# Performance work log

Measured on AMD Instinct MI355X. Metric: run time of the kernel, lower is better.

## Reference

```python
import jax, jax.numpy as jnp
import numpy as np

B, P, C = 2, 512, 21          # images, proposals/image, classes (incl background)
REG = 5                       # xc, yc, w, h, angle(deg)
DET = 100                     # detections_per_img
IMW, IMH = 1024, 800
SCORE_THRESH = 0.05
NMS_THR = 0.5
WEIGHTS = (10.0, 10.0, 5.0, 5.0, 3.0)
BBOX_XFORM_CLIP = float(np.log(1000.0 / 16.0))
MAXV = 8                      # max vertices of quad-quad intersection


def setup_inputs() -> dict:
    key = jax.random.key(0)
    k1, k2, k3 = jax.random.split(key, 3)
    class_logits = jax.random.normal(k1, (B * P, C), jnp.float32)
    box_regression = jax.random.normal(k2, (B * P, C * REG), jnp.float32)
    u = jax.random.uniform(k3, (B * P, 5), jnp.float32)
    rrects = jnp.stack([
        u[:, 0] * IMW,            # xc
        u[:, 1] * IMH,            # yc
        u[:, 2] * 200.0 + 16.0,   # w
        u[:, 3] * 200.0 + 16.0,   # h
        u[:, 4] * 360.0 - 180.0,  # angle in degrees
    ], axis=1)
    return {"class_logits": class_logits, "box_regression": box_regression, "rrects": rrects}


def rect_pts(r):
    # r [..., 5] -> corner points [..., 4, 2] (CCW quad in math coords)
    xc, yc, w, h, ang = (r[..., i] for i in range(5))
    t = ang * (jnp.pi / 180.0)
    c, s = jnp.cos(t), jnp.sin(t)
    dx, dy = w * 0.5, h * 0.5
    ox = jnp.stack([-dx, dx, dx, -dx], -1)
    oy = jnp.stack([-dy, -dy, dy, dy], -1)
    x = xc[..., None] + c[..., None] * ox - s[..., None] * oy
    y = yc[..., None] + s[..., None] * ox + c[..., None] * oy
    return jnp.stack([x, y], -1)


def decode(deltas, anchors):
    # BoxCoder.decode for rotated boxes, weights (wx,wy,ww,wh,wa)
    d = deltas.reshape(-1, C, REG) / jnp.asarray(WEIGHTS, deltas.dtype)
    dx, dy, dw, dh, da = (d[..., i] for i in range(REG))
    dw = jnp.minimum(dw, BBOX_XFORM_CLIP)
    dh = jnp.minimum(dh, BBOX_XFORM_CLIP)
    xc, yc, w, h, a = (anchors[:, i:i + 1] for i in range(5))
    px = dx * w + xc
    py = dy * h + yc
    pw = jnp.exp(dw) * w
    ph = jnp.exp(dh) * h
    pa = da * (180.0 / jnp.pi) + a
    return jnp.stack([px, py, pw, ph, pa], -1)  # [N, C, 5]


def _clip_edge(poly, n, a, b):
    # Sutherland-Hodgman clip of convex poly (buffer [MAXV,2], count n) by halfplane left of a->b
    d = b - a
    out = jnp.zeros((MAXV, 2), poly.dtype)
    m = jnp.int32(0)
    nn = jnp.maximum(n, 1)
    for i in range(MAXV):
        act = i < n
        s = poly[i]
        e = poly[jnp.mod(i + 1, nn)]
        cs = d[0] * (s[1] - a[1]) - d[1] * (s[0] - a[0])
        ce = d[0] * (e[1] - a[1]) - d[1] * (e[0] - a[0])
        denom = cs - ce
        t = cs / jnp.where(jnp.abs(denom) > 1e-12, denom, 1e-12)
        ip = s + t * (e - s)
        s_in = cs >= 0
        e_in = ce >= 0
        app1 = act & (s_in != e_in)           # crossing -> intersection point
        out = out.at[m].set(jnp.where(app1, ip, out[m]))
        m = m + app1.astype(jnp.int32)
        app2 = act & e_in                     # end point inside -> keep it
        out = out.at[m].set(jnp.where(app2, e, out[m]))
        m = m + app2.astype(jnp.int32)
    return out, m


def inter_area(p1, p2):
    # exact intersection area of two convex quads [4,2]
    poly = jnp.zeros((MAXV, 2), p1.dtype).at[:4].set(p1)
    n = jnp.int32(4)
    for k in range(4):
        poly, n = _clip_edge(poly, n, p2[k], p2[(k + 1) % 4])
    idx = jnp.arange(MAXV)
    nn = jnp.maximum(n, 1)
    nxt = jnp.mod(idx + 1, nn)
    cross = poly[:, 0] * poly[nxt, 1] - poly[nxt, 0] * poly[:, 1]
    area = 0.5 * jnp.abs(jnp.sum(jnp.where(idx < n, cross, 0.0)))
    return jnp.where(n >= 3, area, 0.0)


def _nms_one(args):
    # greedy rotated NMS on one (image,class) score-sorted set
    rr, valid = args                       # [P,5], [P] bool (sorted by desc score)
    pts = rect_pts(rr)                     # [P,4,2]
    areas = rr[:, 2] * rr[:, 3]
    inter = jax.vmap(lambda p: jax.vmap(lambda q: inter_area(p, q))(pts))(pts)
    iou = inter / (areas[:, None] + areas[None, :] - inter + 1e-8)
    n = rr.shape[0]
    def body(i, keep):
        sup = jnp.any(keep & (iou[i] > NMS_THR))
        return keep.at[i].set(valid[i] & jnp.logical_not(sup))
    return jax.lax.fori_loop(0, n, body, jnp.zeros((n,), bool))


def reference(class_logits, box_regression, rrects):
    scores = jax.nn.softmax(class_logits, -1)           # [N,C]
    proposals = decode(box_regression, rrects)          # [N,C,5]
    pts = rect_pts(proposals)                           # [N,C,4,2]
    mn, mx = pts.min(-2), pts.max(-2)
    bb = jnp.concatenate([mn, mx], -1)                  # xyxy [N,C,4]
    bb = jnp.stack([
        jnp.clip(bb[..., 0], 0.0, IMW - 1.0),
        jnp.clip(bb[..., 1], 0.0, IMH - 1.0),
        jnp.clip(bb[..., 2], 0.0, IMW - 1.0),
        jnp.clip(bb[..., 3], 0.0, IMH - 1.0),
    ], -1)

    # per-image, foreground classes only; [B, C-1, P, ...]
    sc = scores.reshape(B, P, C)[:, :, 1:].transpose(0, 2, 1)
    pr = proposals.reshape(B, P, C, 5)[:, :, 1:].transpose(0, 2, 1, 3)
    bx = bb.reshape(B, P, C, 4)[:, :, 1:].transpose(0, 2, 1, 3)

    valid = sc > SCORE_THRESH
    masked = jnp.where(valid, sc, -1.0)
    order = jnp.argsort(-masked, axis=-1)               # desc score per class
    sc_s = jnp.take_along_axis(masked, order, -1)
    valid_s = jnp.take_along_axis(valid, order, -1)
    pr_s = jnp.take_along_axis(pr, order[..., None], 2)
    bx_s = jnp.take_along_axis(bx, order[..., None], 2)

    keep = jax.lax.map(_nms_one, (jax.lax.stop_gradient(pr_s).reshape(-1, P, 5),
                                  valid_s.reshape(-1, P))).reshape(B, C - 1, P)
    keep = jax.lax.stop_gradient(keep)

    msk = jnp.where(keep, sc_s, -1.0)
    flat_s = msk.reshape(B, -1)                         # [B,(C-1)*P]
    top_idx = jax.lax.top_k(flat_s, DET)[1]
    sel_s = jnp.take_along_axis(flat_s, top_idx, -1)
    ok = sel_s > 0.0
    sel_bb = jnp.take_along_axis(bx_s.reshape(B, -1, 4), top_idx[..., None], 1)
    sel_rr = jnp.take_along_axis(pr_s.reshape(B, -1, 5), top_idx[..., None], 1)
    lab = jnp.broadcast_to(jnp.arange(1, C, dtype=jnp.int32)[:, None], (C - 1, P)).reshape(-1)
    sel_lab = lab[top_idx]

    out_bb = jnp.where(ok[..., None], sel_bb, 0.0)
    out_rr = jnp.where(ok[..., None], sel_rr, 0.0)
    out_sc = jnp.where(ok, sel_s, 0.0)
    out_lab = jnp.where(ok, sel_lab, 0)
    return out_bb, out_rr, out_sc, out_lab
```

## Files before the change

kernel.cpp:

```cpp
#include <hip/hip_runtime.h>
#include <stdint.h>

#pragma clang fp contract(off)

#define B_ 2
#define P_ 512
#define C_ 21
#define CF 20
#define DET 100
#define SCORE_THRESH 0.05f
#define NMS_THR 0.5f
#define BBOX_CLIP 4.135166556742356f
#define NC (CF * DET)

typedef unsigned long long u64;
typedef unsigned int u32;

__device__ __forceinline__ u32 f2o(float f) {
  u32 u = __float_as_uint(f);
  return (u & 0x80000000u) ? ~u : (u | 0x80000000u);
}
__device__ __forceinline__ float o2f(u32 o) {
  u32 u = (o & 0x80000000u) ? (o ^ 0x80000000u) : ~o;
  return __uint_as_float(u);
}

__global__ void __launch_bounds__(256)
prep_kernel(const float* __restrict__ logits,
            const float* __restrict__ breg,
            const float* __restrict__ rrects,
            float* __restrict__ scsS,
            float* __restrict__ ptsS,
            float* __restrict__ aabbS,
            float* __restrict__ pr5S,
            float* __restrict__ areaS,
            int* __restrict__ gV,
            u64* __restrict__ sup) {
  int g = blockIdx.x;
  int b = g / CF, cf = g % CF, c = cf + 1;
  int tid = threadIdx.x;

  __shared__ u64 lkey[P_];
  __shared__ int cnt;
  if (tid == 0) cnt = 0;

  u64 kreg[2];
  float fx[2][4], fy[2][4];
  float fab[2][4];
  float fp5[2][5];
  float far_[2];
  float fsc[2];
  #pragma unroll
  for (int e = 0; e < 2; ++e) {
    int p = tid + e * 256;
    int n = b * P_ + p;
    const float* lg = logits + n * C_;
    float mx = lg[0];
    for (int k = 1; k < C_; ++k) mx = fmaxf(mx, lg[k]);
    float den = 0.f;
    for (int k = 0; k < C_; ++k) den += expf(lg[k] - mx);
    float sc = expf(lg[c] - mx) / den;

    const float* d = breg + n * (C_ * 5) + c * 5;
    float dx = d[0] / 10.0f, dy = d[1] / 10.0f;
    float dw = d[2] / 5.0f, dh = d[3] / 5.0f, da = d[4] / 3.0f;
    dw = fminf(dw, BBOX_CLIP);
    dh = fminf(dh, BBOX_CLIP);
    const float* an = rrects + n * 5;
    float px = dx * an[2] + an[0];
    float py = dy * an[3] + an[1];
    float pw = expf(dw) * an[2];
    float ph = expf(dh) * an[3];
    float pa = da * 57.29577951308232f + an[4];
    fp5[e][0] = px; fp5[e][1] = py; fp5[e][2] = pw; fp5[e][3] = ph; fp5[e][4] = pa;
    far_[e] = pw * ph;

    float t = pa * 0.017453292519943295f;
    float cs = cosf(t), sn = sinf(t);
    float hx = pw * 0.5f, hy = ph * 0.5f;
    float ox[4] = {-hx, hx, hx, -hx};
    float oy[4] = {-hy, -hy, hy, hy};
    float minx = 1e30f, miny = 1e30f, maxx = -1e30f, maxy = -1e30f;
    #pragma unroll
    for (int qq = 0; qq < 4; ++qq) {
      float x = px + cs * ox[qq] - sn * oy[qq];
      float y = py + sn * ox[qq] + cs * oy[qq];
      fx[e][qq] = x; fy[e][qq] = y;
      minx = fminf(minx, x); maxx = fmaxf(maxx, x);
      miny = fminf(miny, y); maxy = fmaxf(maxy, y);
    }
    fab[e][0] = minx; fab[e][1] = miny; fab[e][2] = maxx; fab[e][3] = maxy;

    bool valid = sc > SCORE_THRESH;
    float v = valid ? sc : -1.0f;
    fsc[e] = v;
    u64 key = ((u64)f2o(v) << 32) | (u32)(~(u32)p);
    lkey[p] = key;
    kreg[e] = key;
    u64 m = __ballot(valid);
    if ((tid & 63) == 0) atomicAdd(&cnt, __popcll(m));
  }
  for (int w = tid; w < P_ * 8; w += 256) sup[(size_t)g * P_ * 8 + w] = 0ull;
  __syncthreads();

  u64 k0 = kreg[0], k1 = kreg[1];
  int r0 = 0, r1 = 0;
  for (int s = 0; s < P_; ++s) {
    u64 ks = lkey[s];
    r0 += (ks > k0) ? 1 : 0;
    r1 += (ks > k1) ? 1 : 0;
  }
  #pragma unroll
  for (int e = 0; e < 2; ++e) {
    if (fsc[e] > 0.f) {
      int r = (e == 0) ? r0 : r1;
      int so = g * P_ + r;
      scsS[so] = fsc[e];
      ((float4*)ptsS)[so * 2]     = make_float4(fx[e][0], fx[e][1], fx[e][2], fx[e][3]);
      ((float4*)ptsS)[so * 2 + 1] = make_float4(fy[e][0], fy[e][1], fy[e][2], fy[e][3]);
      ((float4*)aabbS)[so] = make_float4(fab[e][0], fab[e][1], fab[e][2], fab[e][3]);
      pr5S[so * 5 + 0] = fp5[e][0]; pr5S[so * 5 + 1] = fp5[e][1];
      pr5S[so * 5 + 2] = fp5[e][2]; pr5S[so * 5 + 3] = fp5[e][3];
      pr5S[so * 5 + 4] = fp5[e][4];
      areaS[so] = far_[e];
    }
  }
  if (tid == 0) gV[g] = cnt;
}

__device__ __forceinline__ float inter_area_reg(const float qx[4], const float qy[4],
                                                const float rx[4], const float ry[4]) {
  float px_[8], py_[8];
  #pragma unroll
  for (int t = 0; t < 8; ++t) { px_[t] = (t < 4) ? qx[t] : 0.f; py_[t] = (t < 4) ? qy[t] : 0.f; }
  int n = 4;
  #pragma unroll
  for (int e = 0; e < 4; ++e) {
    float a0 = rx[e], a1 = ry[e];
    float b0 = rx[(e + 1) & 3], b1 = ry[(e + 1) & 3];
    float dx = b0 - a0, dy = b1 - a1;
    float ox_[8], oy_[8];
    #pragma unroll
    for (int t = 0; t < 8; ++t) { ox_[t] = 0.f; oy_[t] = 0.f; }
    float cr[8];
    #pragma unroll
    for (int t = 0; t < 8; ++t) cr[t] = dx * (py_[t] - a1) - dy * (px_[t] - a0);
    int m = 0;
    int nn = (n > 1) ? n : 1;
    #pragma unroll
    for (int t = 0; t < 8; ++t) {
      bool act = t < n;
      float sx = px_[t], sy = py_[t];
      float ex, ey, ce;
      if (t == 7) { ex = px_[0]; ey = py_[0]; ce = cr[0]; }
      else {
        bool wrap = (t + 1 == nn);
        ex = wrap ? px_[0] : px_[t + 1];
        ey = wrap ? py_[0] : py_[t + 1];
        ce = wrap ? cr[0] : cr[t + 1];
      }
      float cs = cr[t];
      float denom = cs - ce;
      float dn = (fabsf(denom) > 1e-12f) ? denom : 1e-12f;
      float tt = cs / dn;
      float ipx = sx + tt * (ex - sx);
      float ipy = sy + tt * (ey - sy);
      bool s_in = cs >= 0.f, e_in = ce >= 0.f;
      bool app1 = act && (s_in != e_in);
      #pragma unroll
      for (int s2 = 0; s2 < 8; ++s2) {
        bool wr = app1 && (m == s2);
        ox_[s2] = wr ? ipx : ox_[s2];
        oy_[s2] = wr ? ipy : oy_[s2];
      }
      m += app1 ? 1 : 0;
      bool app2 = act && e_in;
      #pragma unroll
      for (int s2 = 0; s2 < 8; ++s2) {
        bool wr = app2 && (m == s2);
        ox_[s2] = wr ? ex : ox_[s2];
        oy_[s2] = wr ? ey : oy_[s2];
      }
      m += app2 ? 1 : 0;
    }
    n = m;
    #pragma unroll
    for (int t = 0; t < 8; ++t) { px_[t] = ox_[t]; py_[t] = oy_[t]; }
  }
  int nn = (n > 1) ? n : 1;
  float s = 0.f;
  #pragma unroll
  for (int t = 0; t < 8; ++t) {
    if (t < n) {
      float nx_x, nx_y;
      if (t == 7) { nx_x = px_[0]; nx_y = py_[0]; }
      else {
        bool wrap = (t + 1 == nn);
        nx_x = wrap ? px_[0] : px_[t + 1];
        nx_y = wrap ? py_[0] : py_[t + 1];
      }
      s += px_[t] * nx_y - nx_x * py_[t];
    }
  }
  float area = 0.5f * fabsf(s);
  return (n >= 3) ? area : 0.f;
}

#define PPT 4
#define TPB 256
__global__ void pair_kernel(const int* __restrict__ gV,
                            const float* __restrict__ aabbS,
                            const float* __restrict__ areaS,
                            const float* __restrict__ ptsS,
                            u64* __restrict__ sup) {
  int g = blockIdx.y;
  int V = gV[g];
  int Tp = V * (V - 1) / 2;
  int base = blockIdx.x * (TPB * PPT);
  if (base >= Tp) return;
  __shared__ u32 q[TPB * PPT];
  __shared__ int qn;
  int tid = threadIdx.x;
  if (tid == 0) qn = 0;
  __syncthreads();
  const float4* ab = (const float4*)aabbS;
  for (int t = 0; t < PPT; ++t) {
    int kk = base + t * TPB + tid;
    if (kk >= Tp) break;
    float kf = (float)kk;
    int i = (int)((1.0f + sqrtf(1.0f + 8.0f * kf)) * 0.5f);
    while (i * (i - 1) / 2 > kk) --i;
    while ((i + 1) * i / 2 <= kk) ++i;
    int j = kk - i * (i - 1) / 2;
    float4 bi = ab[g * P_ + i];
    float4 bj = ab[g * P_ + j];
    bool ov = (bi.x <= bj.z) && (bj.x <= bi.z) && (bi.y <= bj.w) && (bj.y <= bi.w);
    if (ov) {
      int s = atomicAdd(&qn, 1);
      q[s] = (u32)((i << 9) | j);
    }
  }
  __syncthreads();
  int nq = qn;
  const float4* pS = (const float4*)ptsS;
  for (int s = tid; s < nq; s += TPB) {
    u32 pk = q[s];
    int i = (int)(pk >> 9), j = (int)(pk & 511);
    float4 ax = pS[(g * P_ + i) * 2];
    float4 ay = pS[(g * P_ + i) * 2 + 1];
    float4 bx = pS[(g * P_ + j) * 2];
    float4 by = pS[(g * P_ + j) * 2 + 1];
    float qx[4] = {ax.x, ax.y, ax.z, ax.w};
    float qy[4] = {ay.x, ay.y, ay.z, ay.w};
    float rx[4] = {bx.x, bx.y, bx.z, bx.w};
    float ry[4] = {by.x, by.y, by.z, by.w};
    float ai = areaS[g * P_ + i];
    float aj = areaS[g * P_ + j];
    float inter = inter_area_reg(qx, qy, rx, ry);
    float iou = inter / (((ai + aj) - inter) + 1e-8f);
    if (iou > NMS_THR)
      atomicOr(&sup[((size_t)g * P_ + i) * 8 + (j >> 6)], 1ull << (j & 63));
  }
}

__global__ void greedy_kernel(const float* __restrict__ scsS, const int* __restrict__ gV,
                              const float* __restrict__ aabbS, const float* __restrict__ pr5S,
                              const u64* __restrict__ sup,
                              u64* __restrict__ cand, float* __restrict__ rec) {
  int g = blockIdx.x;
  int tid = threadIdx.x;
  __shared__ u64 lsup[P_ * 8];
  __shared__ u32 skeep[16];
  int V = gV[g];
  for (int w = tid; w < V * 8; w += 64) lsup[w] = sup[(size_t)g * P_ * 8 + w];
  __syncthreads();
  u64 keepw = 0;
  u64 cur = (tid < 8 && V > 0) ? lsup[tid] : 0ull;
  for (int i = 0; i < V; ++i) {
    u64 nxt = (tid < 8 && (i + 1) < V) ? lsup[(i + 1) * 8 + tid] : 0ull;
    bool supd = __any((cur & keepw) != 0ull);
    if (!supd && tid == (i >> 6)) keepw |= 1ull << (i & 63);
    cur = nxt;
  }
  if (tid < 8) { skeep[tid * 2] = (u32)keepw; skeep[tid * 2 + 1] = (u32)(keepw >> 32); }
  __syncthreads();
  int cls = g % CF;
  int tot = 0;
  #pragma unroll
  for (int t = 0; t < 16; ++t) tot += __popc(skeep[t]);
  for (int r = tid; r < V; r += 64) {
    if ((skeep[r >> 5] >> (r & 31)) & 1u) {
      int slot = __popc(skeep[r >> 5] & ((1u << (r & 31)) - 1u));
      for (int t = 0; t < (r >> 5); ++t) slot += __popc(skeep[t]);
      if (slot < DET) {
        float sv = scsS[g * P_ + r];
        int flat = cls * P_ + r;
        cand[g * DET + slot] = ((u64)f2o(sv) << 32) | (u32)(~(u32)flat);
        int so = g * P_ + r;
        float* rr = rec + (size_t)(g * DET + slot) * 12;
        rr[0] = fminf(fmaxf(aabbS[so * 4 + 0], 0.f), 1023.0f);
        rr[1] = fminf(fmaxf(aabbS[so * 4 + 1], 0.f), 799.0f);
        rr[2] = fminf(fmaxf(aabbS[so * 4 + 2], 0.f), 1023.0f);
        rr[3] = fminf(fmaxf(aabbS[so * 4 + 3], 0.f), 799.0f);
        rr[4] = pr5S[so * 5 + 0]; rr[5] = pr5S[so * 5 + 1]; rr[6] = pr5S[so * 5 + 2];
        rr[7] = pr5S[so * 5 + 3]; rr[8] = pr5S[so * 5 + 4];
        rr[9] = sv;
        rr[10] = (float)(cls + 1);
        rr[11] = 0.f;
      }
    }
  }
  int fill = tot < DET ? tot : DET;
  for (int s = fill + tid; s < DET; s += 64) cand[g * DET + s] = 0ull;
}

__global__ void rank_kernel(const u64* __restrict__ cand, const float* __restrict__ rec,
                            float* __restrict__ out) {
  int b = blockIdx.y;
  int tid = threadIdx.x;
  __shared__ u64 lc[NC];
  __shared__ int ncand;
  if (tid == 0) ncand = 0;
  __syncthreads();
  int nz = 0;
  for (int i = tid; i < NC; i += 256) {
    u64 v = cand[b * NC + i];
    lc[i] = v;
    nz += (v != 0ull) ? 1 : 0;
  }
  u64 m = __ballot(nz > 0);
  if (nz > 0) atomicAdd(&ncand, nz);
  (void)m;
  __syncthreads();
  int ci = blockIdx.x * 256 + tid;
  if (ci >= NC) return;
  if (blockIdx.x == 0 && tid < DET && tid >= ncand) {
    int o_bb = (b * DET + tid) * 4;
    int o_rr = B_ * DET * 4 + (b * DET + tid) * 5;
    int o_sc = B_ * DET * 9 + b * DET + tid;
    int o_lab = B_ * DET * 10 + b * DET + tid;
    out[o_bb + 0] = 0.f; out[o_bb + 1] = 0.f; out[o_bb + 2] = 0.f; out[o_bb + 3] = 0.f;
    out[o_rr + 0] = 0.f; out[o_rr + 1] = 0.f; out[o_rr + 2] = 0.f;
    out[o_rr + 3] = 0.f; out[o_rr + 4] = 0.f;
    out[o_sc] = 0.f;
    out[o_lab] = 0.f;
  }
  u64 k = lc[ci];
  if (k == 0ull) return;
  int rank = 0;
  #pragma unroll
  for (int gp = 0; gp < CF; ++gp) {
    int lo = 0, hi = DET;
    while (lo < hi) {
      int mid = (lo + hi) >> 1;
      if (lc[gp * DET + mid] > k) lo = mid + 1; else hi = mid;
    }
    rank += lo;
  }
  if (rank >= DET) return;
  const float* rr = rec + (size_t)(b * NC + ci) * 12;
  int o_bb = (b * DET + rank) * 4;
  int o_rr = B_ * DET * 4 + (b * DET + rank) * 5;
  int o_sc = B_ * DET * 9 + b * DET + rank;
  int o_lab = B_ * DET * 10 + b * DET + rank;
  out[o_bb + 0] = rr[0]; out[o_bb + 1] = rr[1];
  out[o_bb + 2] = rr[2]; out[o_bb + 3] = rr[3];
  out[o_rr + 0] = rr[4]; out[o_rr + 1] = rr[5]; out[o_rr + 2] = rr[6];
  out[o_rr + 3] = rr[7]; out[o_rr + 4] = rr[8];
  out[o_sc] = rr[9];
  out[o_lab] = rr[10];
}

extern "C" void kernel_launch(void* const* d_in, const int* in_sizes, int n_in,
                              void* d_out, int out_size, void* d_ws, size_t ws_size,
                              hipStream_t stream) {
  const float* logits = (const float*)d_in[0];
  const float* breg   = (const float*)d_in[1];
  const float* rrects = (const float*)d_in[2];
  float* out = (float*)d_out;

  const int G = B_ * CF;
  u64*   sup  = (u64*)d_ws;
  u64*   cand = sup + (size_t)G * P_ * 8;
  int*   gV   = (int*)(cand + G * DET);
  float* scsS = (float*)(gV + 64);
  float* ptsS = scsS + (size_t)G * P_;
  float* aabbS = ptsS + (size_t)G * P_ * 8;
  float* pr5S = aabbS + (size_t)G * P_ * 4;
  float* areaS = pr5S + (size_t)G * P_ * 5;
  float* rec  = areaS + (size_t)G * P_;

  prep_kernel<<<G, 256, 0, stream>>>(logits, breg, rrects,
                                     scsS, ptsS, aabbS, pr5S, areaS, gV, sup);
  pair_kernel<<<dim3(128, G), TPB, 0, stream>>>(gV, aabbS, areaS, ptsS, sup);
  greedy_kernel<<<G, 64, 0, stream>>>(scsS, gV, aabbS, pr5S, sup, cand, rec);
  rank_kernel<<<dim3((NC + 255) / 256, B_), 256, 0, stream>>>(cand, rec, out);
}
```

Baseline: 133.4 us.

## Fuse four NMS kernels into one cooperative kernel with grid syncs

```diff
diff --git a/kernel.cpp b/kernel.cpp
--- a/kernel.cpp
+++ b/kernel.cpp
@@ -1,4 +1,5 @@
 #include <hip/hip_runtime.h>
+#include <hip/hip_cooperative_groups.h>
 #include <stdint.h>
 
 #pragma clang fp contract(off)
@@ -7,14 +8,19 @@
 #define P_ 512
 #define C_ 21
 #define CF 20
+#define G_ (B_ * CF)
 #define DET 100
 #define SCORE_THRESH 0.05f
 #define NMS_THR 0.5f
 #define BBOX_CLIP 4.135166556742356f
 #define NC (CF * DET)
+#define GRID 256
+#define TPB 256
 
 typedef unsigned long long u64;
 typedef unsigned int u32;
+
+namespace cg = cooperative_groups;
 
 __device__ __forceinline__ u32 f2o(float f) {
   u32 u = __float_as_uint(f);
@@ -23,109 +29,6 @@
 __device__ __forceinline__ float o2f(u32 o) {
   u32 u = (o & 0x80000000u) ? (o ^ 0x80000000u) : ~o;
   return __uint_as_float(u);
-}
-
-__global__ void __launch_bounds__(256)
-prep_kernel(const float* __restrict__ logits,
-            const float* __restrict__ breg,
-            const float* __restrict__ rrects,
-            float* __restrict__ scsS,
-            float* __restrict__ ptsS,
-            float* __restrict__ aabbS,
-            float* __restrict__ pr5S,
-            float* __restrict__ areaS,
-            int* __restrict__ gV,
-            u64* __restrict__ sup) {
-  int g = blockIdx.x;
-  int b = g / CF, cf = g % CF, c = cf + 1;
-  int tid = threadIdx.x;
-
-  __shared__ u64 lkey[P_];
-  __shared__ int cnt;
-  if (tid == 0) cnt = 0;
-
-  u64 kreg[2];
-  float fx[2][4], fy[2][4];
-  float fab[2][4];
-  float fp5[2][5];
-  float far_[2];
-  float fsc[2];
-  #pragma unroll
-  for (int e = 0; e < 2; ++e) {
-    int p = tid + e * 256;
-    int n = b * P_ + p;
-    const float* lg = logits + n * C_;
-    float mx = lg[0];
-    for (int k = 1; k < C_; ++k) mx = fmaxf(mx, lg[k]);
-    float den = 0.f;
-    for (int k = 0; k < C_; ++k) den += expf(lg[k] - mx);
-    float sc = expf(lg[c] - mx) / den;
-
-    const float* d = breg + n * (C_ * 5) + c * 5;
-    float dx = d[0] / 10.0f, dy = d[1] / 10.0f;
-    float dw = d[2] / 5.0f, dh = d[3] / 5.0f, da = d[4] / 3.0f;
-    dw = fminf(dw, BBOX_CLIP);
-    dh = fminf(dh, BBOX_CLIP);
-    const float* an = rrects + n * 5;
-    float px = dx * an[2] + an[0];
-    float py = dy * an[3] + an[1];
-    float pw = expf(dw) * an[2];
-    float ph = expf(dh) * an[3];
-    float pa = da * 57.29577951308232f + an[4];
-    fp5[e][0] = px; fp5[e][1] = py; fp5[e][2] = pw; fp5[e][3] = ph; fp5[e][4] = pa;
-    far_[e] = pw * ph;
-
-    float t = pa * 0.017453292519943295f;
-    float cs = cosf(t), sn = sinf(t);
-    float hx = pw * 0.5f, hy = ph * 0.5f;
-    float ox[4] = {-hx, hx, hx, -hx};
-    float oy[4] = {-hy, -hy, hy, hy};
-    float minx = 1e30f, miny = 1e30f, maxx = -1e30f, maxy = -1e30f;
-    #pragma unroll
-    for (int qq = 0; qq < 4; ++qq) {
-      float x = px + cs * ox[qq] - sn * oy[qq];
-      float y = py + sn * ox[qq] + cs * oy[qq];
-      fx[e][qq] = x; fy[e][qq] = y;
-      minx = fminf(minx, x); maxx = fmaxf(maxx, x);
-      miny = fminf(miny, y); maxy = fmaxf(maxy, y);
-    }
-    fab[e][0] = minx; fab[e][1] = miny; fab[e][2] = maxx; fab[e][3] = maxy;
-
-    bool valid = sc > SCORE_THRESH;
-    float v = valid ? sc : -1.0f;
-    fsc[e] = v;
-    u64 key = ((u64)f2o(v) << 32) | (u32)(~(u32)p);
-    lkey[p] = key;
-    kreg[e] = key;
-    u64 m = __ballot(valid);
-    if ((tid & 63) == 0) atomicAdd(&cnt, __popcll(m));
-  }
-  for (int w = tid; w < P_ * 8; w += 256) sup[(size_t)g * P_ * 8 + w] = 0ull;
-  __syncthreads();
-
-  u64 k0 = kreg[0], k1 = kreg[1];
-  int r0 = 0, r1 = 0;
-  for (int s = 0; s < P_; ++s) {
-    u64 ks = lkey[s];
-    r0 += (ks > k0) ? 1 : 0;
-    r1 += (ks > k1) ? 1 : 0;
-  }
-  #pragma unroll
-  for (int e = 0; e < 2; ++e) {
-    if (fsc[e] > 0.f) {
-      int r = (e == 0) ? r0 : r1;
-      int so = g * P_ + r;
-      scsS[so] = fsc[e];
-      ((float4*)ptsS)[so * 2]     = make_float4(fx[e][0], fx[e][1], fx[e][2], fx[e][3]);
-      ((float4*)ptsS)[so * 2 + 1] = make_float4(fy[e][0], fy[e][1], fy[e][2], fy[e][3]);
-      ((float4*)aabbS)[so] = make_float4(fab[e][0], fab[e][1], fab[e][2], fab[e][3]);
-      pr5S[so * 5 + 0] = fp5[e][0]; pr5S[so * 5 + 1] = fp5[e][1];
-      pr5S[so * 5 + 2] = fp5[e][2]; pr5S[so * 5 + 3] = fp5[e][3];
-      pr5S[so * 5 + 4] = fp5[e][4];
-      areaS[so] = far_[e];
-    }
-  }
-  if (tid == 0) gV[g] = cnt;
 }
 
 __device__ __forceinline__ float inter_area_reg(const float qx[4], const float qy[4],
@@ -206,169 +109,274 @@
   return (n >= 3) ? area : 0.f;
 }
 
-#define PPT 4
-#define TPB 256
-__global__ void pair_kernel(const int* __restrict__ gV,
-                            const float* __restrict__ aabbS,
-                            const float* __restrict__ areaS,
-                            const float* __restrict__ ptsS,
-                            u64* __restrict__ sup) {
-  int g = blockIdx.y;
-  int V = gV[g];
-  int Tp = V * (V - 1) / 2;
-  int base = blockIdx.x * (TPB * PPT);
-  if (base >= Tp) return;
-  __shared__ u32 q[TPB * PPT];
-  __shared__ int qn;
+__global__ void __launch_bounds__(256, 1)
+fused_kernel(const float* __restrict__ logits,
+             const float* __restrict__ breg,
+             const float* __restrict__ rrects,
+             u64* __restrict__ lkeyG,
+             float* __restrict__ scsS,
+             float* __restrict__ ptsS,
+             float* __restrict__ aabbS,
+             float* __restrict__ pr5S,
+             float* __restrict__ areaS,
+             int* __restrict__ gV,
+             u64* __restrict__ sup,
+             u64* __restrict__ cand,
+             float* __restrict__ rec,
+             float* __restrict__ out) {
+  cg::grid_group grid = cg::this_grid();
   int tid = threadIdx.x;
-  if (tid == 0) qn = 0;
-  __syncthreads();
-  const float4* ab = (const float4*)aabbS;
-  for (int t = 0; t < PPT; ++t) {
-    int kk = base + t * TPB + tid;
-    if (kk >= Tp) break;
-    float kf = (float)kk;
-    int i = (int)((1.0f + sqrtf(1.0f + 8.0f * kf)) * 0.5f);
-    while (i * (i - 1) / 2 > kk) --i;
-    while ((i + 1) * i / 2 <= kk) ++i;
-    int j = kk - i * (i - 1) / 2;
-    float4 bi = ab[g * P_ + i];
-    float4 bj = ab[g * P_ + j];
-    bool ov = (bi.x <= bj.z) && (bj.x <= bi.z) && (bi.y <= bj.w) && (bj.y <= bi.w);
-    if (ov) {
-      int s = atomicAdd(&qn, 1);
-      q[s] = (u32)((i << 9) | j);
-    }
-  }
-  __syncthreads();
-  int nq = qn;
-  const float4* pS = (const float4*)ptsS;
-  for (int s = tid; s < nq; s += TPB) {
-    u32 pk = q[s];
-    int i = (int)(pk >> 9), j = (int)(pk & 511);
-    float4 ax = pS[(g * P_ + i) * 2];
-    float4 ay = pS[(g * P_ + i) * 2 + 1];
-    float4 bx = pS[(g * P_ + j) * 2];
-    float4 by = pS[(g * P_ + j) * 2 + 1];
-    float qx[4] = {ax.x, ax.y, ax.z, ax.w};
-    float qy[4] = {ay.x, ay.y, ay.z, ay.w};
-    float rx[4] = {bx.x, bx.y, bx.z, bx.w};
-    float ry[4] = {by.x, by.y, by.z, by.w};
-    float ai = areaS[g * P_ + i];
-    float aj = areaS[g * P_ + j];
-    float inter = inter_area_reg(qx, qy, rx, ry);
-    float iou = inter / (((ai + aj) - inter) + 1e-8f);
-    if (iou > NMS_THR)
-      atomicOr(&sup[((size_t)g * P_ + i) * 8 + (j >> 6)], 1ull << (j & 63));
-  }
-}
-
-__global__ void greedy_kernel(const float* __restrict__ scsS, const int* __restrict__ gV,
-                              const float* __restrict__ aabbS, const float* __restrict__ pr5S,
-                              const u64* __restrict__ sup,
-                              u64* __restrict__ cand, float* __restrict__ rec) {
-  int g = blockIdx.x;
-  int tid = threadIdx.x;
-  __shared__ u64 lsup[P_ * 8];
-  __shared__ u32 skeep[16];
-  int V = gV[g];
-  for (int w = tid; w < V * 8; w += 64) lsup[w] = sup[(size_t)g * P_ * 8 + w];
-  __syncthreads();
-  u64 keepw = 0;
-  u64 cur = (tid < 8 && V > 0) ? lsup[tid] : 0ull;
-  for (int i = 0; i < V; ++i) {
-    u64 nxt = (tid < 8 && (i + 1) < V) ? lsup[(i + 1) * 8 + tid] : 0ull;
-    bool supd = __any((cur & keepw) != 0ull);
-    if (!supd && tid == (i >> 6)) keepw |= 1ull << (i & 63);
-    cur = nxt;
-  }
-  if (tid < 8) { skeep[tid * 2] = (u32)keepw; skeep[tid * 2 + 1] = (u32)(keepw >> 32); }
-  __syncthreads();
-  int cls = g % CF;
-  int tot = 0;
-  #pragma unroll
-  for (int t = 0; t < 16; ++t) tot += __popc(skeep[t]);
-  for (int r = tid; r < V; r += 64) {
-    if ((skeep[r >> 5] >> (r & 31)) & 1u) {
-      int slot = __popc(skeep[r >> 5] & ((1u << (r & 31)) - 1u));
-      for (int t = 0; t < (r >> 5); ++t) slot += __popc(skeep[t]);
-      if (slot < DET) {
-        float sv = scsS[g * P_ + r];
-        int flat = cls * P_ + r;
-        cand[g * DET + slot] = ((u64)f2o(sv) << 32) | (u32)(~(u32)flat);
-        int so = g * P_ + r;
-        float* rr = rec + (size_t)(g * DET + slot) * 12;
-        rr[0] = fminf(fmaxf(aabbS[so * 4 + 0], 0.f), 1023.0f);
-        rr[1] = fminf(fmaxf(aabbS[so * 4 + 1], 0.f), 799.0f);
-        rr[2] = fminf(fmaxf(aabbS[so * 4 + 2], 0.f), 1023.0f);
-        rr[3] = fminf(fmaxf(aabbS[so * 4 + 3], 0.f), 799.0f);
-        rr[4] = pr5S[so * 5 + 0]; rr[5] = pr5S[so * 5 + 1]; rr[6] = pr5S[so * 5 + 2];
-        rr[7] = pr5S[so * 5 + 3]; rr[8] = pr5S[so * 5 + 4];
-        rr[9] = sv;
-        rr[10] = (float)(cls + 1);
-        rr[11] = 0.f;
-      }
-    }
-  }
-  int fill = tot < DET ? tot : DET;
-  for (int s = fill + tid; s < DET; s += 64) cand[g * DET + s] = 0ull;
-}
-
-__global__ void rank_kernel(const u64* __restrict__ cand, const float* __restrict__ rec,
-                            float* __restrict__ out) {
-  int b = blockIdx.y;
-  int tid = threadIdx.x;
-  __shared__ u64 lc[NC];
-  __shared__ int ncand;
-  if (tid == 0) ncand = 0;
-  __syncthreads();
-  int nz = 0;
-  for (int i = tid; i < NC; i += 256) {
-    u64 v = cand[b * NC + i];
-    lc[i] = v;
-    nz += (v != 0ull) ? 1 : 0;
-  }
-  u64 m = __ballot(nz > 0);
-  if (nz > 0) atomicAdd(&ncand, nz);
-  (void)m;
-  __syncthreads();
-  int ci = blockIdx.x * 256 + tid;
-  if (ci >= NC) return;
-  if (blockIdx.x == 0 && tid < DET && tid >= ncand) {
-    int o_bb = (b * DET + tid) * 4;
-    int o_rr = B_ * DET * 4 + (b * DET + tid) * 5;
-    int o_sc = B_ * DET * 9 + b * DET + tid;
-    int o_lab = B_ * DET * 10 + b * DET + tid;
-    out[o_bb + 0] = 0.f; out[o_bb + 1] = 0.f; out[o_bb + 2] = 0.f; out[o_bb + 3] = 0.f;
-    out[o_rr + 0] = 0.f; out[o_rr + 1] = 0.f; out[o_rr + 2] = 0.f;
-    out[o_rr + 3] = 0.f; out[o_rr + 4] = 0.f;
-    out[o_sc] = 0.f;
-    out[o_lab] = 0.f;
-  }
-  u64 k = lc[ci];
-  if (k == 0ull) return;
-  int rank = 0;
-  #pragma unroll
-  for (int gp = 0; gp < CF; ++gp) {
-    int lo = 0, hi = DET;
-    while (lo < hi) {
-      int mid = (lo + hi) >> 1;
-      if (lc[gp * DET + mid] > k) lo = mid + 1; else hi = mid;
-    }
-    rank += lo;
-  }
-  if (rank >= DET) return;
-  const float* rr = rec + (size_t)(b * NC + ci) * 12;
-  int o_bb = (b * DET + rank) * 4;
-  int o_rr = B_ * DET * 4 + (b * DET + rank) * 5;
-  int o_sc = B_ * DET * 9 + b * DET + rank;
-  int o_lab = B_ * DET * 10 + b * DET + rank;
-  out[o_bb + 0] = rr[0]; out[o_bb + 1] = rr[1];
-  out[o_bb + 2] = rr[2]; out[o_bb + 3] = rr[3];
-  out[o_rr + 0] = rr[4]; out[o_rr + 1] = rr[5]; out[o_rr + 2] = rr[6];
-  out[o_rr + 3] = rr[7]; out[o_rr + 4] = rr[8];
-  out[o_sc] = rr[9];
-  out[o_lab] = rr[10];
+  int gid = blockIdx.x * TPB + tid;
+
+  __shared__ u64 shbuf[P_ * 8 + 16];
+
+  for (int w = gid; w < G_ * P_ * 8; w += GRID * TPB) sup[w] = 0ull;
+
+  float fx[4], fy[4], fab[4], fp5[5], farea = 0.f, fsc = -1.0f;
+  u64 mykey = 0;
+  int g = 0, p = 0;
+  bool active = gid < G_ * P_;
+  if (active) {
+    g = gid >> 9; p = gid & (P_ - 1);
+    int b = g / CF, cf = g % CF, c = cf + 1;
+    int n = b * P_ + p;
+    const float* lg = logits + n * C_;
+    float mx = lg[0];
+    for (int k = 1; k < C_; ++k) mx = fmaxf(mx, lg[k]);
+    float den = 0.f;
+    for (int k = 0; k < C_; ++k) den += expf(lg[k] - mx);
+    float sc = expf(lg[c] - mx) / den;
+
+    const float* d = breg + n * (C_ * 5) + c * 5;
+    float dxx = d[0] / 10.0f, dyy = d[1] / 10.0f;
+    float dw = d[2] / 5.0f, dh = d[3] / 5.0f, da = d[4] / 3.0f;
+    dw = fminf(dw, BBOX_CLIP);
+    dh = fminf(dh, BBOX_CLIP);
+    const float* an = rrects + n * 5;
+    float px = dxx * an[2] + an[0];
+    float py = dyy * an[3] + an[1];
+    float pw = expf(dw) * an[2];
+    float ph = expf(dh) * an[3];
+    float pa = da * 57.29577951308232f + an[4];
+    fp5[0] = px; fp5[1] = py; fp5[2] = pw; fp5[3] = ph; fp5[4] = pa;
+    farea = pw * ph;
+
+    float t = pa * 0.017453292519943295f;
+    float cs = cosf(t), sn = sinf(t);
+    float hx = pw * 0.5f, hy = ph * 0.5f;
+    float ox[4] = {-hx, hx, hx, -hx};
+    float oy[4] = {-hy, -hy, hy, hy};
+    float minx = 1e30f, miny = 1e30f, maxx = -1e30f, maxy = -1e30f;
+    #pragma unroll
+    for (int qq = 0; qq < 4; ++qq) {
+      float x = px + cs * ox[qq] - sn * oy[qq];
+      float y = py + sn * ox[qq] + cs * oy[qq];
+      fx[qq] = x; fy[qq] = y;
+      minx = fminf(minx, x); maxx = fmaxf(maxx, x);
+      miny = fminf(miny, y); maxy = fmaxf(maxy, y);
+    }
+    fab[0] = minx; fab[1] = miny; fab[2] = maxx; fab[3] = maxy;
+
+    bool valid = sc > SCORE_THRESH;
+    fsc = valid ? sc : -1.0f;
+    mykey = ((u64)f2o(fsc) << 32) | (u32)(~(u32)p);
+    lkeyG[gid] = mykey;
+  }
+  __threadfence();
+  grid.sync();
+
+  if (blockIdx.x < (G_ * P_) / TPB) {
+    u64* keys = shbuf;
+    int g2 = (blockIdx.x * TPB) >> 9;
+    for (int i = tid; i < P_; i += TPB) keys[i] = lkeyG[g2 * P_ + i];
+    __syncthreads();
+    u64 k = mykey;
+    int rank = 0, V = 0;
+    for (int s = 0; s < P_; ++s) {
+      u64 ks = keys[s];
+      rank += (ks > k) ? 1 : 0;
+      V += ((u32)(ks >> 32) > 0x80000000u) ? 1 : 0;
+    }
+    if (p == 0) gV[g] = V;
+    if (fsc > 0.f) {
+      int so = g * P_ + rank;
+      scsS[so] = fsc;
+      ((float4*)ptsS)[so * 2]     = make_float4(fx[0], fx[1], fx[2], fx[3]);
+      ((float4*)ptsS)[so * 2 + 1] = make_float4(fy[0], fy[1], fy[2], fy[3]);
+      ((float4*)aabbS)[so] = make_float4(fab[0], fab[1], fab[2], fab[3]);
+      pr5S[so * 5 + 0] = fp5[0]; pr5S[so * 5 + 1] = fp5[1];
+      pr5S[so * 5 + 2] = fp5[2]; pr5S[so * 5 + 3] = fp5[3];
+      pr5S[so * 5 + 4] = fp5[4];
+      areaS[so] = farea;
+    }
+  }
+  __threadfence();
+  grid.sync();
+
+  {
+    u32* q = (u32*)shbuf;
+    int* qn = (int*)(shbuf + 512);
+    const float4* ab = (const float4*)aabbS;
+    const float4* pS = (const float4*)ptsS;
+    for (int u = blockIdx.x; u < G_ * 128; u += GRID) {
+      int g3 = u >> 7, cch = u & 127;
+      int V = gV[g3];
+      int Tp = V * (V - 1) / 2;
+      int base = cch * 1024;
+      if (base >= Tp) continue;
+      if (tid == 0) *qn = 0;
+      __syncthreads();
+      #pragma unroll
+      for (int t = 0; t < 4; ++t) {
+        int kk = base + t * TPB + tid;
+        if (kk >= Tp) break;
+        float kf = (float)kk;
+        int i = (int)((1.0f + sqrtf(1.0f + 8.0f * kf)) * 0.5f);
+        while (i * (i - 1) / 2 > kk) --i;
+        while ((i + 1) * i / 2 <= kk) ++i;
+        int j = kk - i * (i - 1) / 2;
+        float4 bi = ab[g3 * P_ + i];
+        float4 bj = ab[g3 * P_ + j];
+        bool ov = (bi.x <= bj.z) && (bj.x <= bi.z) && (bi.y <= bj.w) && (bj.y <= bi.w);
+        if (ov) {
+          int s = atomicAdd(qn, 1);
+          q[s] = (u32)((i << 9) | j);
+        }
+      }
+      __syncthreads();
+      int nq = *qn;
+      for (int s = tid; s < nq; s += TPB) {
+        u32 pk = q[s];
+        int i = (int)(pk >> 9), j = (int)(pk & 511);
+        float4 ax = pS[(g3 * P_ + i) * 2];
+        float4 ay = pS[(g3 * P_ + i) * 2 + 1];
+        float4 bx = pS[(g3 * P_ + j) * 2];
+        float4 by = pS[(g3 * P_ + j) * 2 + 1];
+        float qx[4] = {ax.x, ax.y, ax.z, ax.w};
+        float qy[4] = {ay.x, ay.y, ay.z, ay.w};
+        float rx[4] = {bx.x, bx.y, bx.z, bx.w};
+        float ry[4] = {by.x, by.y, by.z, by.w};
+        float ai = areaS[g3 * P_ + i];
+        float aj = areaS[g3 * P_ + j];
+        float inter = inter_area_reg(qx, qy, rx, ry);
+        float iou = inter / (((ai + aj) - inter) + 1e-8f);
+        if (iou > NMS_THR)
+          atomicOr(&sup[((size_t)g3 * P_ + i) * 8 + (j >> 6)], 1ull << (j & 63));
+      }
+      __syncthreads();
+    }
+  }
+  __threadfence();
+  grid.sync();
+
+  if (blockIdx.x < G_) {
+    u64* lsup = shbuf;
+    u32* skeep = (u32*)(shbuf + P_ * 8);
+    int g4 = blockIdx.x;
+    int V = gV[g4];
+    for (int w = tid; w < V * 8; w += TPB) lsup[w] = sup[(size_t)g4 * P_ * 8 + w];
+    __syncthreads();
+    if (tid < 64) {
+      u64 keepw = 0;
+      u64 cur = (tid < 8 && V > 0) ? lsup[tid] : 0ull;
+      for (int i = 0; i < V; ++i) {
+        u64 nxt = (tid < 8 && (i + 1) < V) ? lsup[(i + 1) * 8 + tid] : 0ull;
+        bool supd = __any((cur & keepw) != 0ull);
+        if (!supd && tid == (i >> 6)) keepw |= 1ull << (i & 63);
+        cur = nxt;
+      }
+      if (tid < 8) { skeep[tid * 2] = (u32)keepw; skeep[tid * 2 + 1] = (u32)(keepw >> 32); }
+    }
+    __syncthreads();
+    int cls = g4 % CF;
+    int tot = 0;
+    #pragma unroll
+    for (int t = 0; t < 16; ++t) tot += __popc(skeep[t]);
+    for (int r = tid; r < V; r += TPB) {
+      if ((skeep[r >> 5] >> (r & 31)) & 1u) {
+        int slot = __popc(skeep[r >> 5] & ((1u << (r & 31)) - 1u));
+        for (int t = 0; t < (r >> 5); ++t) slot += __popc(skeep[t]);
+        if (slot < DET) {
+          float sv = scsS[g4 * P_ + r];
+          int flat = cls * P_ + r;
+          cand[g4 * DET + slot] = ((u64)f2o(sv) << 32) | (u32)(~(u32)flat);
+          int so = g4 * P_ + r;
+          float* rr = rec + (size_t)(g4 * DET + slot) * 12;
+          rr[0] = fminf(fmaxf(aabbS[so * 4 + 0], 0.f), 1023.0f);
+          rr[1] = fminf(fmaxf(aabbS[so * 4 + 1], 0.f), 799.0f);
+          rr[2] = fminf(fmaxf(aabbS[so * 4 + 2], 0.f), 1023.0f);
+          rr[3] = fminf(fmaxf(aabbS[so * 4 + 3], 0.f), 799.0f);
+          rr[4] = pr5S[so * 5 + 0]; rr[5] = pr5S[so * 5 + 1]; rr[6] = pr5S[so * 5 + 2];
+          rr[7] = pr5S[so * 5 + 3]; rr[8] = pr5S[so * 5 + 4];
+          rr[9] = sv;
+          rr[10] = (float)(cls + 1);
+          rr[11] = 0.f;
+        }
+      }
+    }
+    int fill = tot < DET ? tot : DET;
+    for (int s = fill + tid; s < DET; s += TPB) cand[g4 * DET + s] = 0ull;
+  }
+  __threadfence();
+  grid.sync();
+
+  if (blockIdx.x < 16) {
+    u64* lc = shbuf;
+    int* ncand = (int*)(shbuf + NC);
+    int b5 = blockIdx.x >> 3;
+    int cbase = (blockIdx.x & 7) * TPB;
+    if (tid == 0) *ncand = 0;
+    __syncthreads();
+    int nz = 0;
+    for (int i = tid; i < NC; i += TPB) {
+      u64 v = cand[b5 * NC + i];
+      lc[i] = v;
+      nz += (v != 0ull) ? 1 : 0;
+    }
+    if (nz > 0) atomicAdd(ncand, nz);
+    __syncthreads();
+    int nc = *ncand;
+    if ((blockIdx.x & 7) == 0 && tid < DET && tid >= nc) {
+      int o_bb = (b5 * DET + tid) * 4;
+      int o_rr = B_ * DET * 4 + (b5 * DET + tid) * 5;
+      int o_sc = B_ * DET * 9 + b5 * DET + tid;
+      int o_lab = B_ * DET * 10 + b5 * DET + tid;
+      out[o_bb + 0] = 0.f; out[o_bb + 1] = 0.f; out[o_bb + 2] = 0.f; out[o_bb + 3] = 0.f;
+      out[o_rr + 0] = 0.f; out[o_rr + 1] = 0.f; out[o_rr + 2] = 0.f;
+      out[o_rr + 3] = 0.f; out[o_rr + 4] = 0.f;
+      out[o_sc] = 0.f;
+      out[o_lab] = 0.f;
+    }
+    int ci = cbase + tid;
+    if (ci < NC) {
+      u64 k = lc[ci];
+      if (k != 0ull) {
+        int rank = 0;
+        #pragma unroll
+        for (int gp = 0; gp < CF; ++gp) {
+          int lo = 0, hi = DET;
+          while (lo < hi) {
+            int mid = (lo + hi) >> 1;
+            if (lc[gp * DET + mid] > k) lo = mid + 1; else hi = mid;
+          }
+          rank += lo;
+        }
+        if (rank < DET) {
+          const float* rr = rec + (size_t)(b5 * NC + ci) * 12;
+          int o_bb = (b5 * DET + rank) * 4;
+          int o_rr = B_ * DET * 4 + (b5 * DET + rank) * 5;
+          int o_sc = B_ * DET * 9 + b5 * DET + rank;
+          int o_lab = B_ * DET * 10 + b5 * DET + rank;
+          out[o_bb + 0] = rr[0]; out[o_bb + 1] = rr[1];
+          out[o_bb + 2] = rr[2]; out[o_bb + 3] = rr[3];
+          out[o_rr + 0] = rr[4]; out[o_rr + 1] = rr[5]; out[o_rr + 2] = rr[6];
+          out[o_rr + 3] = rr[7]; out[o_rr + 4] = rr[8];
+          out[o_sc] = rr[9];
+          out[o_lab] = rr[10];
+        }
+      }
+    }
+  }
 }
 
 extern "C" void kernel_launch(void* const* d_in, const int* in_sizes, int n_in,
@@ -379,20 +387,22 @@
   const float* rrects = (const float*)d_in[2];
   float* out = (float*)d_out;
 
-  const int G = B_ * CF;
-  u64*   sup  = (u64*)d_ws;
-  u64*   cand = sup + (size_t)G * P_ * 8;
-  int*   gV   = (int*)(cand + G * DET);
-  float* scsS = (float*)(gV + 64);
-  float* ptsS = scsS + (size_t)G * P_;
-  float* aabbS = ptsS + (size_t)G * P_ * 8;
-  float* pr5S = aabbS + (size_t)G * P_ * 4;
-  float* areaS = pr5S + (size_t)G * P_ * 5;
-  float* rec  = areaS + (size_t)G * P_;
-
-  prep_kernel<<<G, 256, 0, stream>>>(logits, breg, rrects,
-                                     scsS, ptsS, aabbS, pr5S, areaS, gV, sup);
-  pair_kernel<<<dim3(128, G), TPB, 0, stream>>>(gV, aabbS, areaS, ptsS, sup);
-  greedy_kernel<<<G, 64, 0, stream>>>(scsS, gV, aabbS, pr5S, sup, cand, rec);
-  rank_kernel<<<dim3((NC + 255) / 256, B_), 256, 0, stream>>>(cand, rec, out);
+  u64*   sup   = (u64*)d_ws;
+  u64*   cand  = sup + (size_t)G_ * P_ * 8;
+  u64*   lkeyG = cand + G_ * DET;
+  int*   gV    = (int*)(lkeyG + (size_t)G_ * P_);
+  float* scsS  = (float*)(gV + 64);
+  float* ptsS  = scsS + (size_t)G_ * P_;
+  float* aabbS = ptsS + (size_t)G_ * P_ * 8;
+  float* pr5S  = aabbS + (size_t)G_ * P_ * 4;
+  float* areaS = pr5S + (size_t)G_ * P_ * 5;
+  float* rec   = areaS + (size_t)G_ * P_;
+
+  void* kargs[] = {
+    (void*)&logits, (void*)&breg, (void*)&rrects,
+    (void*)&lkeyG, (void*)&scsS, (void*)&ptsS, (void*)&aabbS, (void*)&pr5S,
+    (void*)&areaS, (void*)&gV, (void*)&sup, (void*)&cand, (void*)&rec, (void*)&out
+  };
+  hipLaunchCooperativeKernel((const void*)fused_kernel, dim3(GRID), dim3(TPB),
+                             kargs, 0, stream);
 }
```

Result: slower. 463.4 us (+247.4%).
